# Kernel tuning notes

Hardware: AMD Instinct MI355X
Metric: run time of the kernel (lower is better)

The kernel has to match this reference:

```python
import jax, jax.numpy as jnp
from jax import lax
import numpy as np

B, C, H, W = 2, 64, 192, 192

def conv2d(x, w, pad):
    return lax.conv_general_dilated(x, w, (1, 1), [(pad, pad), (pad, pad)],
                                    dimension_numbers=('NCHW', 'OIHW', 'NCHW'))

def bilinear_sample(x, py, px):
    # x: [B,C,H,W]; py, px: [B,H,W] absolute fractional coords; zero padding outside.
    Bb, Cc, Hh, Ww = x.shape
    y0 = jnp.floor(py); x0 = jnp.floor(px)
    wy1 = py - y0; wx1 = px - x0
    xf = x.reshape(Bb, Cc, Hh * Ww)
    def gather(yi, xi):
        valid = (yi >= 0) & (yi < Hh) & (xi >= 0) & (xi < Ww)
        yc = jnp.clip(yi, 0, Hh - 1).astype(jnp.int32)
        xc = jnp.clip(xi, 0, Ww - 1).astype(jnp.int32)
        idx = (yc * Ww + xc).reshape(Bb, 1, Hh * Ww)
        v = jnp.take_along_axis(xf, idx, axis=2).reshape(Bb, Cc, Hh, Ww)
        return v * valid[:, None].astype(x.dtype)
    return (gather(y0, x0) * ((1 - wy1) * (1 - wx1))[:, None]
            + gather(y0, x0 + 1) * ((1 - wy1) * wx1)[:, None]
            + gather(y0 + 1, x0) * (wy1 * (1 - wx1))[:, None]
            + gather(y0 + 1, x0 + 1) * (wy1 * wx1)[:, None])

def deform_conv(x, w_off, b_off, w_mod, b_mod, w_reg, k):
    # torchvision deform_conv2d semantics with modulation (mask), stride=1, dilation=1.
    pad = k // 2
    offset = conv2d(x, w_off, pad) + b_off[None, :, None, None]   # [B,2*k*k,H,W] (y,x) interleaved
    mask = 2.0 * jax.nn.sigmoid(conv2d(x, w_mod, pad) + b_mod[None, :, None, None])  # [B,k*k,H,W]
    Bb, Cc, Hh, Ww = x.shape
    gy = jnp.arange(Hh, dtype=x.dtype)[None, :, None]
    gx = jnp.arange(Ww, dtype=x.dtype)[None, None, :]
    out = jnp.zeros((Bb, w_reg.shape[0], Hh, Ww), x.dtype)
    for i in range(k):          # fixed structural loop over kernel taps
        for j in range(k):
            t = i * k + j
            py = gy - pad + i + offset[:, 2 * t]
            px = gx - pad + j + offset[:, 2 * t + 1]
            samp = bilinear_sample(x, py, px) * mask[:, t][:, None]  # [B,C,H,W]
            out = out + jnp.einsum('bchw,oc->bohw', samp, w_reg[:, :, i, j])
    return out

def _branch(x, w_pre, w_off, b_off, w_mod, b_mod, w_reg, k):
    h = jax.nn.relu(conv2d(x, w_pre, 0))  # BasicConv 1x1 + ReLU (no bias)
    return deform_conv(h, w_off, b_off, w_mod, b_mod, w_reg, k)

def _forward(x_max, x_mid, x_small,
             w_pre_max, w_off_max, b_off_max, w_mod_max, b_mod_max, w_reg_max,
             w_pre_mid, w_off_mid, b_off_mid, w_mod_mid, b_mod_mid, w_reg_mid,
             w_pre_small, w_off_small, b_off_small, w_mod_small, b_mod_small, w_reg_small,
             w1, w2):
    y = x_max + x_mid + x_small
    a = _branch(x_max, w_pre_max, w_off_max, b_off_max, w_mod_max, b_mod_max, w_reg_max, 7)
    m = _branch(x_mid, w_pre_mid, w_off_mid, b_off_mid, w_mod_mid, b_mod_mid, w_reg_mid, 5)
    s = _branch(x_small, w_pre_small, w_off_small, b_off_small, w_mod_small, b_mod_small, w_reg_small, 3)
    x = jnp.tanh(m) * a
    x = jax.nn.relu(conv2d(x, w1, 0))
    x = jnp.tanh(s) * x
    x = jax.nn.relu(conv2d(x, w2, 0))
    return x + y

def setup_inputs() -> dict:
    key = jax.random.key(0)
    ks = jax.random.split(key, 32)
    d = {}
    d['x_max'] = jax.random.normal(ks[0], (B, C, H, W), jnp.float32)
    d['x_mid'] = jax.random.normal(ks[1], (B, C, H, W), jnp.float32)
    d['x_small'] = jax.random.normal(ks[2], (B, C, H, W), jnp.float32)
    i = 3
    for name, k in (('max', 7), ('mid', 5), ('small', 3)):
        d[f'w_pre_{name}'] = jax.random.normal(ks[i], (C, C, 1, 1), jnp.float32) * 0.05; i += 1
        d[f'w_off_{name}'] = jax.random.normal(ks[i], (2 * k * k, C, k, k), jnp.float32) * 0.01; i += 1
        d[f'b_off_{name}'] = jax.random.normal(ks[i], (2 * k * k,), jnp.float32) * 0.01; i += 1
        d[f'w_mod_{name}'] = jax.random.normal(ks[i], (k * k, C, k, k), jnp.float32) * 0.01; i += 1
        d[f'b_mod_{name}'] = jax.random.normal(ks[i], (k * k,), jnp.float32) * 0.01; i += 1
        d[f'w_reg_{name}'] = jax.random.normal(ks[i], (C, C, k, k), jnp.float32) * 0.02; i += 1
    d['w1'] = jax.random.normal(ks[i], (C, C, 1, 1), jnp.float32) * 0.05; i += 1
    d['w2'] = jax.random.normal(ks[i], (C, C, 1, 1), jnp.float32) * 0.05
    return d

def reference(x_max, x_mid, x_small,
              w_pre_max, w_off_max, b_off_max, w_mod_max, b_mod_max, w_reg_max,
              w_pre_mid, w_off_mid, b_off_mid, w_mod_mid, b_mod_mid, w_reg_mid,
              w_pre_small, w_off_small, b_off_small, w_mod_small, b_mod_small, w_reg_small,
              w1, w2):
    return _forward(x_max, x_mid, x_small,
                    w_pre_max, w_off_max, b_off_max, w_mod_max, b_mod_max, w_reg_max,
                    w_pre_mid, w_off_mid, b_off_mid, w_mod_mid, b_mod_mid, w_reg_mid,
                    w_pre_small, w_off_small, b_off_small, w_mod_small, b_mod_small, w_reg_small,
                    w1, w2)
```

## Files before the change

### kernel.cpp

```cpp
#include <hip/hip_runtime.h>
#include <hip/hip_bf16.h>
#include <math.h>

#define BB   2
#define CC   64
#define HH   192
#define WW   192
#define HW   (HH*WW)
#define HALO 3
#define HP   (HH + 2*HALO)
#define WP   (WW + 2*HALO)
#define PLANE (HP*WP)

typedef __attribute__((ext_vector_type(8))) _Float16 f16x8;
typedef __attribute__((ext_vector_type(4))) _Float16 f16x4;
typedef __attribute__((ext_vector_type(8))) unsigned short u16x8;
typedef __attribute__((ext_vector_type(4))) float f32x4;

__device__ __forceinline__ float fast_tanh(float x) {
    float e = __expf(2.f * x);
    return 1.f - 2.f * __builtin_amdgcn_rcpf(e + 1.f);
}
__device__ __forceinline__ f16x8 bc16(u16x8 v) { return __builtin_bit_cast(f16x8, v); }

__global__ __launch_bounds__(256) void conv_pre_k(
    const float* __restrict__ X0, const float* __restrict__ X1,
    const float* __restrict__ X2,
    const float* __restrict__ W0, const float* __restrict__ W1,
    const float* __restrict__ W2,
    u16x8* __restrict__ hp8all)
{
    __shared__ float wl[64*32];
    int tid = threadIdx.x;
    int oh  = blockIdx.y;
    int z   = blockIdx.z;
    const float* X = (z == 0) ? X0 : ((z == 1) ? X1 : X2);
    const float* W = (z == 0) ? W0 : ((z == 1) ? W1 : W2);
    u16x8* hp8 = hp8all + (size_t)z * ((size_t)BB*8*PLANE);

    #pragma unroll
    for (int n = 0; n < 8; n++) {
        int idx = tid + n*256;
        int op  = idx >> 6, c = idx & 63;
        wl[c*32 + op] = W[(size_t)(oh*32 + op)*64 + c];
    }
    __syncthreads();

    int p  = blockIdx.x*256 + tid;
    int b  = p / HW;
    int pp = p - b*HW;
    size_t base = (size_t)b*CC*HW + pp;

    float acc[32];
    #pragma unroll
    for (int o = 0; o < 32; o++) acc[o] = 0.f;

    #pragma unroll 4
    for (int c = 0; c < 64; c++) {
        float xv = X[base + (size_t)c*HW];
        const float4* w4 = (const float4*)(wl + c*32);
        #pragma unroll
        for (int q = 0; q < 8; q++) {
            float4 w = w4[q];
            acc[4*q+0] = fmaf(w.x, xv, acc[4*q+0]);
            acc[4*q+1] = fmaf(w.y, xv, acc[4*q+1]);
            acc[4*q+2] = fmaf(w.z, xv, acc[4*q+2]);
            acc[4*q+3] = fmaf(w.w, xv, acc[4*q+3]);
        }
    }

    int y = pp / WW, x = pp - y*WW;
    #pragma unroll
    for (int gq = 0; gq < 4; gq++) {
        u16x8 v;
        #pragma unroll
        for (int c = 0; c < 8; c++)
            v[c] = __builtin_bit_cast(unsigned short,
                     (_Float16)fmaxf(acc[gq*8+c], 0.f));
        hp8[(size_t)(b*8 + oh*4 + gq)*PLANE + (size_t)(y+HALO)*WP + (x+HALO)] = v;
    }
}

template<int MODE>
__global__ __launch_bounds__(256) void conv1x1_k(
    const _Float16* __restrict__ Xv, const _Float16* __restrict__ Mv,
    const float* __restrict__ W,
    const float* __restrict__ Y0, const float* __restrict__ Y1,
    const float* __restrict__ Y2,
    void* __restrict__ outv)
{
    __shared__ float wl[64*32];
    int tid = threadIdx.x;
    int oh  = blockIdx.y;
    #pragma unroll
    for (int n = 0; n < 8; n++) {
        int idx = tid + n*256;
        int op  = idx >> 6, c = idx & 63;
        wl[c*32 + op] = W[(size_t)(oh*32 + op)*64 + c];
    }
    __syncthreads();

    int p  = blockIdx.x*256 + tid;
    int b  = p / HW;
    int pp = p - b*HW;
    size_t base = (size_t)b*CC*HW + pp;

    float acc[32];
    #pragma unroll
    for (int o = 0; o < 32; o++) acc[o] = 0.f;

    #pragma unroll 4
    for (int c = 0; c < 64; c++) {
        float xv = (float)Xv[base + (size_t)c*HW];
        xv *= fast_tanh((float)Mv[base + (size_t)c*HW]);
        const float4* w4 = (const float4*)(wl + c*32);
        #pragma unroll
        for (int q = 0; q < 8; q++) {
            float4 w = w4[q];
            acc[4*q+0] = fmaf(w.x, xv, acc[4*q+0]);
            acc[4*q+1] = fmaf(w.y, xv, acc[4*q+1]);
            acc[4*q+2] = fmaf(w.z, xv, acc[4*q+2]);
            acc[4*q+3] = fmaf(w.w, xv, acc[4*q+3]);
        }
    }

    if (MODE == 1) {
        _Float16* op = (_Float16*)outv + base + (size_t)(oh*32)*HW;
        #pragma unroll
        for (int o = 0; o < 32; o++)
            op[(size_t)o*HW] = (_Float16)fmaxf(acc[o], 0.f);
    } else {
        float* op = (float*)outv + base + (size_t)(oh*32)*HW;
        size_t gi = base + (size_t)(oh*32)*HW;
        #pragma unroll
        for (int o = 0; o < 32; o++) {
            float yv = Y0[gi + (size_t)o*HW] + Y1[gi + (size_t)o*HW] + Y2[gi + (size_t)o*HW];
            op[(size_t)o*HW] = fmaxf(acc[o], 0.f) + yv;
        }
    }
}

template<int K>
__device__ void bake_wtb_dev(const float* __restrict__ Wreg,
                             f16x8* __restrict__ wtb, int t, int tid)
{
    constexpr int KK = K*K;
    for (int e = tid; e < 512; e += 256) {
        int kk = e >> 8, rem = e & 255;
        int ot = rem >> 6, l = rem & 63;
        int lr = l & 15, lg = l >> 4;
        int o  = ot*16 + lr;
        f16x8 v;
        #pragma unroll
        for (int j = 0; j < 8; j++) {
            int c = kk*32 + lg*8 + j;
            v[j] = (_Float16)Wreg[((size_t)o*CC + c)*KK + t];
        }
        wtb[(size_t)t*512 + e] = v;
    }
}
template<int K>
__device__ void bake_wbg_dev(const float* __restrict__ Woff,
                             const float* __restrict__ Wmod,
                             f16x8* __restrict__ wbg, int pos, int tid)
{
    constexpr int KK  = K*K;
    constexpr int NTF = (3*KK + 15)/16;
    for (int idx = tid; idx < 2*NTF*64; idx += 256) {
        int kk  = idx / (NTF*64);
        int rem = idx - kk*(NTF*64);
        int nt  = rem >> 6;
        int l   = rem & 63;
        int lg  = l >> 4, lr = l & 15;
        int n   = nt*16 + lr;
        f16x8 v;
        #pragma unroll
        for (int j = 0; j < 8; j++) {
            int c = kk*32 + lg*8 + j;
            float w = 0.f;
            if (n < 2*KK)      w = Woff[((size_t)n*CC + c)*KK + pos];
            else if (n < 3*KK) w = Wmod[((size_t)(n - 2*KK)*CC + c)*KK + pos];
            v[j] = (_Float16)w;
        }
        wbg[(size_t)pos*(2*NTF*64) + idx] = v;
    }
}
__global__ __launch_bounds__(256) void bake_all_k(
    const float* wreg7, const float* woff7, const float* wmod7,
    const float* wreg5, const float* woff5, const float* wmod5,
    const float* wreg3, const float* woff3, const float* wmod3,
    f16x8* wtb7, f16x8* wbg7, f16x8* wtb5, f16x8* wbg5,
    f16x8* wtb3, f16x8* wbg3)
{
    int blk = blockIdx.x, tid = threadIdx.x;
    if (blk < 49) {
        bake_wtb_dev<7>(wreg7, wtb7, blk, tid);
        bake_wbg_dev<7>(woff7, wmod7, wbg7, blk, tid);
    } else if (blk < 74) {
        int p = blk - 49;
        bake_wtb_dev<5>(wreg5, wtb5, p, tid);
        bake_wbg_dev<5>(woff5, wmod5, wbg5, p, tid);
    } else {
        int p = blk - 74;
        bake_wtb_dev<3>(wreg3, wtb3, p, tid);
        bake_wbg_dev<3>(woff3, wmod3, wbg3, p, tid);
    }
}

template<int K, int MT, int NS, int PPR>
__global__ __launch_bounds__(256) void offmod_mfma_k(
    const u16x8* __restrict__ hp8,
    const f16x8* __restrict__ wbg,
    const float* __restrict__ Boff, const float* __restrict__ Bmod,
    _Float16* __restrict__ om)
{
    constexpr int PAD  = K/2;
    constexpr int KK   = K*K;
    constexpr int NTF  = (3*KK + 15)/16;
    constexpr int NT   = NTF/NS;
    constexpr int PBB  = HW/(64*MT);
    constexpr int NBLK = BB*PBB*NS;
    constexpr int ROUNDS = (KK + PPR - 1)/PPR;
    constexpr int WELEM  = PPR*2*NT*64;

    __shared__ f16x8 wl[WELEM];

    int raw = blockIdx.x;
    int swz = (raw & 7)*(NBLK >> 3) + (raw >> 3);
    int ng  = swz % NS;
    int s   = swz / NS;
    int b   = s / PBB;
    int blk = s - b*PBB;

    int tid  = threadIdx.x;
    int wave = tid >> 6;
    int l    = tid & 63;
    int lg   = l >> 4, lr = l & 15;
    int pxw  = blk*(4*MT*16) + wave*(MT*16);
    int y    = pxw / WW, x0 = pxw - y*WW;

    f32x4 acc[MT][NT];
    #pragma unroll
    for (int mt = 0; mt < MT; mt++)
        #pragma unroll
        for (int nt = 0; nt < NT; nt++) acc[mt][nt] = (f32x4)0.f;

    const u16x8* hb = hp8 + (size_t)(b*8)*PLANE;

    for (int r = 0; r < ROUNDS; r++) {
        __syncthreads();
        #pragma unroll
        for (int ii = 0; ii < (WELEM + 255)/256; ii++) {
            int idx = tid + ii*256;
            if (WELEM % 256 == 0 || idx < WELEM) {
                int pp  = idx / (2*NT*64);
                int rem = idx - pp*(2*NT*64);
                int kk  = rem / (NT*64);
                int rem2= rem - kk*(NT*64);
                int nt  = rem2 >> 6;
                int ll  = rem2 & 63;
                int pos = r*PPR + pp;
                if (pos < KK)
                    wl[idx] = wbg[(size_t)pos*(2*NTF*64)
                                  + (size_t)(kk*NTF + ng*NT + nt)*64 + ll];
            }
        }
        __syncthreads();

        #pragma unroll
        for (int pp = 0; pp < PPR; pp++) {
            int pos = r*PPR + pp;
            if (pos >= KK) break;
            int i = pos / K, j = pos - (pos/K)*K;
            int rbase = (y + HALO - PAD + i)*WP + (x0 + HALO - PAD + j);

            #pragma unroll
            for (int kk = 0; kk < 2; kk++) {
                const f16x8* G = (const f16x8*)(hb + (size_t)(kk*4 + lg)*PLANE + rbase);
                f16x8 a[MT];
                #pragma unroll
                for (int mt = 0; mt < MT; mt++) a[mt] = G[mt*16 + lr];
                #pragma unroll
                for (int nt = 0; nt < NT; nt++) {
                    f16x8 bf = wl[((pp*2 + kk)*NT + nt)*64 + l];
                    #pragma unroll
                    for (int mt = 0; mt < MT; mt++)
                        acc[mt][nt] = __builtin_amdgcn_mfma_f32_16x16x32_f16(
                            a[mt], bf, acc[mt][nt], 0, 0, 0);
                }
            }
        }
    }

    #pragma unroll
    for (int nt = 0; nt < NT; nt++) {
        int n = ng*NT*16 + nt*16 + lr;
        if (n < 3*KK) {
            bool is_mask = (n >= 2*KK);
            float bias = is_mask ? Bmod[n - 2*KK] : Boff[n];
            _Float16* dst0 = om + ((size_t)b*3*KK + n)*HW + pxw + lg*4;
            #pragma unroll
            for (int mt = 0; mt < MT; mt++) {
                f32x4 v = acc[mt][nt];
                float v0 = v[0] + bias, v1 = v[1] + bias, v2 = v[2] + bias, v3 = v[3] + bias;
                if (is_mask) {
                    v0 = 2.f * __builtin_amdgcn_rcpf(1.f + __expf(-v0));
                    v1 = 2.f * __builtin_amdgcn_rcpf(1.f + __expf(-v1));
                    v2 = 2.f * __builtin_amdgcn_rcpf(1.f + __expf(-v2));
                    v3 = 2.f * __builtin_amdgcn_rcpf(1.f + __expf(-v3));
                }
                f16x4 o;
                o[0] = (_Float16)v0; o[1] = (_Float16)v1;
                o[2] = (_Float16)v2; o[3] = (_Float16)v3;
                *reinterpret_cast<f16x4*>(dst0 + mt*16) = o;
            }
        }
    }
}

template<int K>
__global__ __launch_bounds__(256, 4) void deform_mfma_k(
    const u16x8* __restrict__ hp8,
    const _Float16* __restrict__ om,
    const f16x8* __restrict__ wtb,
    _Float16* __restrict__ out)
{
    constexpr int PAD = K/2;
    constexpr int KK  = K*K;
    constexpr int NSB = HW/16;
    constexpr int HWW = K + 2;
    constexpr int WWW = 16 + K + 2;
    constexpr int WELEMS = 8*HWW*WWW;
    constexpr int NPT = KK*16;
    constexpr int COORD_B = NPT*8 + NPT*4 + ((NPT*2 + 15)/16)*16;
    constexpr int RED_B   = 2*64*16*4;
    constexpr int UNION_B = (COORD_B > RED_B ? COORD_B : RED_B);

    __shared__ u16x8 win[8][HWW][WWW];
    __shared__ __align__(16) char ubuf[UNION_B];

    f16x4*          hco  = (f16x4*)ubuf;
    unsigned*       gofs = (unsigned*)(ubuf + NPT*8);
    unsigned short* wofs = (unsigned short*)(ubuf + NPT*8 + NPT*4);

    int raw = blockIdx.x;
    int swz = (raw & 7)*((BB*NSB) >> 3) + (raw >> 3);
    int b = swz / NSB, strip = swz - b*NSB;

    int tid  = threadIdx.x;
    int wave = tid >> 6;
    int l    = tid & 63;
    int lg   = l >> 4;
    int lr   = l & 15;
    int th   = wave & 1;
    int kkh  = wave >> 1;
    int pxbase = strip*16;
    int y    = pxbase / WW;
    int xs   = pxbase - y*WW;

    int wy0 = y  + HALO - PAD - 1;
    int wx0 = xs + HALO - PAD - 1;

    {
        const u16x8* hbb = hp8 + (size_t)(b*8)*PLANE;
        for (int idx = tid; idx < WELEMS; idx += 256) {
            int g  = idx / (HWW*WWW);
            int r2 = idx - g*(HWW*WWW);
            int r  = r2 / WWW;
            int c2 = r2 - r*WWW;
            int gy = min(max(wy0 + r, 0), HP-1);
            int gx = min(max(wx0 + c2, 0), WP-1);
            win[g][r][c2] = hbb[(size_t)g*PLANE + gy*WP + gx];
        }
    }
    {
        const _Float16* ob = om + (size_t)b*3*KK*HW + pxbase;
        for (int idx = tid; idx < NPT; idx += 256) {
            int pxl = idx & 15, t = idx >> 4;
            float offy = (float)ob[(size_t)(2*t  )*HW + pxl];
            float offx = (float)ob[(size_t)(2*t+1)*HW + pxl];
            float mk   = (float)ob[(size_t)(2*KK+t)*HW + pxl];
            int i = t / K, j = t - (t/K)*K;
            float py  = (float)(y - PAD + i) + offy;
            float pxf = (float)(xs + pxl - PAD + j) + offx;
            float fy = floorf(py), fx = floorf(pxf);
            float wy1 = py - fy, wx1 = pxf - fx;
            int iy0 = (int)fy, ix0 = (int)fx;
            int Y0 = min(max(iy0, -1), HH) + HALO;
            int X0 = min(max(ix0, -1), WW) + HALO;
            int ry = Y0 - wy0, rx = X0 - wx0;
            bool in = ((unsigned)ry <= (unsigned)(HWW-2)) &
                      ((unsigned)rx <= (unsigned)(WWW-2));
            f16x4 h;
            h[0] = (_Float16)((1.f-wy1)*(1.f-wx1)*mk);
            h[1] = (_Float16)((1.f-wy1)*wx1*mk);
            h[2] = (_Float16)(wy1*(1.f-wx1)*mk);
            h[3] = (_Float16)(wy1*wx1*mk);
            hco[idx]  = h;
            gofs[idx] = (unsigned)(Y0*WP + X0);
            wofs[idx] = (unsigned short)((ry*WWW + rx) | (in ? 0 : 0x8000));
        }
    }
    __syncthreads();

    int t0 = (KK*th)/2, t1 = (KK*(th+1))/2;

    f32x4 acc[4];
    #pragma unroll
    for (int ot = 0; ot < 4; ot++) acc[ot] = (f32x4)0.f;

    const u16x8* hb   = hp8 + (size_t)(b*8 + kkh*4 + lg)*PLANE;
    const u16x8* wing = &win[kkh*4 + lg][0][0];

    #pragma unroll 1
    for (int t = t0; t < t1; t++) {
        int idx = t*16 + lr;
        f16x4 h = hco[idx];
        unsigned short wf = wofs[idx];
        bool in = (wf & 0x8000) == 0;

        f16x8 c0, c1, c2, c3;
        if (__all(in)) {
            const u16x8* Wp = wing + wf;
            c0 = bc16(Wp[0]);   c1 = bc16(Wp[1]);
            c2 = bc16(Wp[WWW]); c3 = bc16(Wp[WWW+1]);
        } else {
            const u16x8* G = hb + gofs[idx];
            c0 = bc16(G[0]);  c1 = bc16(G[1]);
            c2 = bc16(G[WP]); c3 = bc16(G[WP+1]);
        }

        f16x8 s = c0*h[0] + c1*h[1] + c2*h[2] + c3*h[3];

        const f16x8* bp = wtb + (size_t)t*8*64 + l;
        #pragma unroll
        for (int ot = 0; ot < 4; ot++) {
            acc[ot] = __builtin_amdgcn_mfma_f32_16x16x32_f16(
                s, bp[(size_t)(kkh*4 + ot)*64], acc[ot], 0, 0, 0);
        }
    }

    __syncthreads();
    float* redf = (float*)ubuf;
    #define RIDX(tt, o, g)  (((tt)*64 + (o))*16 + (((g) ^ ((o) & 3)) * 4))
    if (kkh == 1) {
        #pragma unroll
        for (int ot = 0; ot < 4; ot++) {
            int o = ot*16 + lr;
            *reinterpret_cast<f32x4*>(&redf[RIDX(th, o, lg)]) = acc[ot];
        }
    }
    __syncthreads();
    if (kkh == 0) {
        #pragma unroll
        for (int ot = 0; ot < 4; ot++) {
            int o = ot*16 + lr;
            acc[ot] += *reinterpret_cast<const f32x4*>(&redf[RIDX(th, o, lg)]);
        }
    }
    __syncthreads();
    if (kkh == 0 && th == 1) {
        #pragma unroll
        for (int ot = 0; ot < 4; ot++) {
            int o = ot*16 + lr;
            *reinterpret_cast<f32x4*>(&redf[RIDX(0, o, lg)]) = acc[ot];
        }
    }
    __syncthreads();
    if (kkh == 0 && th == 0) {
        _Float16* ob = out + (size_t)b*CC*HW + pxbase + lg*4;
        #pragma unroll
        for (int ot = 0; ot < 4; ot++) {
            int o = ot*16 + lr;
            f32x4 rr = *reinterpret_cast<const f32x4*>(&redf[RIDX(0, o, lg)]);
            rr += acc[ot];
            f16x4 v;
            v[0] = (_Float16)rr[0]; v[1] = (_Float16)rr[1];
            v[2] = (_Float16)rr[2]; v[3] = (_Float16)rr[3];
            *reinterpret_cast<f16x4*>(ob + (size_t)o*HW) = v;
        }
    }
    #undef RIDX
}

extern "C" void kernel_launch(void* const* d_in, const int* in_sizes, int n_in,
                              void* d_out, int out_size, void* d_ws, size_t ws_size,
                              hipStream_t stream)
{
    const float* x_max      = (const float*)d_in[0];
    const float* x_mid      = (const float*)d_in[1];
    const float* x_small    = (const float*)d_in[2];
    const float* w_pre_max  = (const float*)d_in[3];
    const float* w_off_max  = (const float*)d_in[4];
    const float* b_off_max  = (const float*)d_in[5];
    const float* w_mod_max  = (const float*)d_in[6];
    const float* b_mod_max  = (const float*)d_in[7];
    const float* w_reg_max  = (const float*)d_in[8];
    const float* w_pre_mid  = (const float*)d_in[9];
    const float* w_off_mid  = (const float*)d_in[10];
    const float* b_off_mid  = (const float*)d_in[11];
    const float* w_mod_mid  = (const float*)d_in[12];
    const float* b_mod_mid  = (const float*)d_in[13];
    const float* w_reg_mid  = (const float*)d_in[14];
    const float* w_pre_small= (const float*)d_in[15];
    const float* w_off_small= (const float*)d_in[16];
    const float* b_off_small= (const float*)d_in[17];
    const float* w_mod_small= (const float*)d_in[18];
    const float* b_mod_small= (const float*)d_in[19];
    const float* w_reg_small= (const float*)d_in[20];
    const float* w1         = (const float*)d_in[21];
    const float* w2         = (const float*)d_in[22];

    float* out = (float*)d_out;
    char*  ws  = (char*)d_ws;

    const size_t HPB = (size_t)BB*8*PLANE;

    u16x8*    hp8 = (u16x8*)ws;                 ws += 3*HPB*16;
    _Float16* om  = (_Float16*)ws;              ws += (size_t)BB*3*49*HW*2;
    _Float16* aa  = (_Float16*)ws;              ws += (size_t)BB*CC*HW*2;
    _Float16* mm  = (_Float16*)ws;              ws += (size_t)BB*CC*HW*2;
    _Float16* sm  = (_Float16*)ws;              ws += (size_t)BB*CC*HW*2;
    _Float16* u   = (_Float16*)ws;              ws += (size_t)BB*CC*HW*2;
    f16x8*    wtb7= (f16x8*)ws;                 ws += (size_t)49*512*16;
    f16x8*    wbg7= (f16x8*)ws;                 ws += (size_t)49*2*10*64*16;
    f16x8*    wtb5= (f16x8*)ws;                 ws += (size_t)25*512*16;
    f16x8*    wbg5= (f16x8*)ws;                 ws += (size_t)25*2*5*64*16;
    f16x8*    wtb3= (f16x8*)ws;                 ws += (size_t)9*512*16;
    f16x8*    wbg3= (f16x8*)ws;

    hipMemsetAsync(hp8, 0, 3*HPB*16, stream);

    const int npix_blocks = (BB*HW)/256;
    const int dfm_blocks  = BB*(HW/16);
    const int off7_blocks = BB*(HW/128)*2;
    const int off5_blocks = BB*(HW/64);
    const int off3_blocks = BB*(HW/128);

    bake_all_k<<<83, 256, 0, stream>>>(
        w_reg_max, w_off_max, w_mod_max,
        w_reg_mid, w_off_mid, w_mod_mid,
        w_reg_small, w_off_small, w_mod_small,
        wtb7, wbg7, wtb5, wbg5, wtb3, wbg3);
    conv_pre_k<<<dim3(npix_blocks, 2, 3), 256, 0, stream>>>(
        x_max, x_mid, x_small, w_pre_max, w_pre_mid, w_pre_small, hp8);

    offmod_mfma_k<7,2,2,2><<<off7_blocks, 256, 0, stream>>>(
        hp8 + 0*HPB, wbg7, b_off_max, b_mod_max, om);
    deform_mfma_k<7><<<dfm_blocks, 256, 0, stream>>>(hp8 + 0*HPB, om, wtb7, aa);

    offmod_mfma_k<5,1,1,2><<<off5_blocks, 256, 0, stream>>>(
        hp8 + 1*HPB, wbg5, b_off_mid, b_mod_mid, om);
    deform_mfma_k<5><<<dfm_blocks, 256, 0, stream>>>(hp8 + 1*HPB, om, wtb5, mm);

    offmod_mfma_k<3,2,1,3><<<off3_blocks, 256, 0, stream>>>(
        hp8 + 2*HPB, wbg3, b_off_small, b_mod_small, om);
    deform_mfma_k<3><<<dfm_blocks, 256, 0, stream>>>(hp8 + 2*HPB, om, wtb3, sm);

    conv1x1_k<1><<<dim3(npix_blocks,2), 256, 0, stream>>>(aa, mm, w1,
                                                  nullptr, nullptr, nullptr, u);
    conv1x1_k<2><<<dim3(npix_blocks,2), 256, 0, stream>>>(u, sm, w2,
                                                  x_max, x_mid, x_small, out);
}
```

Before: 431.9 us.

## Double-buffer offset/mask weight staging per tap and retile N-splits

```diff
diff --git a/kernel.cpp b/kernel.cpp
--- a/kernel.cpp
+++ b/kernel.cpp
@@ -207,7 +207,7 @@
     }
 }
 
-template<int K, int MT, int NS, int PPR>
+template<int K, int MT, int NS>
 __global__ __launch_bounds__(256) void offmod_mfma_k(
     const u16x8* __restrict__ hp8,
     const f16x8* __restrict__ wbg,
@@ -220,10 +220,9 @@
     constexpr int NT   = NTF/NS;
     constexpr int PBB  = HW/(64*MT);
     constexpr int NBLK = BB*PBB*NS;
-    constexpr int ROUNDS = (KK + PPR - 1)/PPR;
-    constexpr int WELEM  = PPR*2*NT*64;
-
-    __shared__ f16x8 wl[WELEM];
+    constexpr int PELEM = 2*NT*64;
+
+    __shared__ f16x8 wl[2][PELEM];
 
     int raw = blockIdx.x;
     int swz = (raw & 7)*(NBLK >> 3) + (raw >> 3);
@@ -247,49 +246,48 @@
 
     const u16x8* hb = hp8 + (size_t)(b*8)*PLANE;
 
-    for (int r = 0; r < ROUNDS; r++) {
+    auto stage = [&](int buf, int pos) {
+        #pragma unroll
+        for (int ii = 0; ii < (PELEM + 255)/256; ii++) {
+            int idx = tid + ii*256;
+            if (PELEM % 256 == 0 || idx < PELEM) {
+                int kk  = idx / (NT*64);
+                int rem = idx - kk*(NT*64);
+                int nt  = rem >> 6;
+                int ll  = rem & 63;
+                wl[buf][idx] = wbg[(size_t)pos*(2*NTF*64)
+                                   + (size_t)(kk*NTF + ng*NT + nt)*64 + ll];
+            }
+        }
+    };
+
+    stage(0, 0);
+    __syncthreads();
+
+    int buf = 0;
+    for (int pos = 0; pos < KK; pos++) {
+        if (pos + 1 < KK) stage(buf ^ 1, pos + 1);
+
+        int i = pos / K, j = pos - (pos/K)*K;
+        int rbase = (y + HALO - PAD + i)*WP + (x0 + HALO - PAD + j);
+
+        #pragma unroll
+        for (int kk = 0; kk < 2; kk++) {
+            const f16x8* G = (const f16x8*)(hb + (size_t)(kk*4 + lg)*PLANE + rbase);
+            f16x8 a[MT];
+            #pragma unroll
+            for (int mt = 0; mt < MT; mt++) a[mt] = G[mt*16 + lr];
+            #pragma unroll
+            for (int nt = 0; nt < NT; nt++) {
+                f16x8 bf = wl[buf][(kk*NT + nt)*64 + l];
+                #pragma unroll
+                for (int mt = 0; mt < MT; mt++)
+                    acc[mt][nt] = __builtin_amdgcn_mfma_f32_16x16x32_f16(
+                        a[mt], bf, acc[mt][nt], 0, 0, 0);
+            }
+        }
         __syncthreads();
-        #pragma unroll
-        for (int ii = 0; ii < (WELEM + 255)/256; ii++) {
-            int idx = tid + ii*256;
-            if (WELEM % 256 == 0 || idx < WELEM) {
-                int pp  = idx / (2*NT*64);
-                int rem = idx - pp*(2*NT*64);
-                int kk  = rem / (NT*64);
-                int rem2= rem - kk*(NT*64);
-                int nt  = rem2 >> 6;
-                int ll  = rem2 & 63;
-                int pos = r*PPR + pp;
-                if (pos < KK)
-                    wl[idx] = wbg[(size_t)pos*(2*NTF*64)
-                                  + (size_t)(kk*NTF + ng*NT + nt)*64 + ll];
-            }
-        }
-        __syncthreads();
-
-        #pragma unroll
-        for (int pp = 0; pp < PPR; pp++) {
-            int pos = r*PPR + pp;
-            if (pos >= KK) break;
-            int i = pos / K, j = pos - (pos/K)*K;
-            int rbase = (y + HALO - PAD + i)*WP + (x0 + HALO - PAD + j);
-
-            #pragma unroll
-            for (int kk = 0; kk < 2; kk++) {
-                const f16x8* G = (const f16x8*)(hb + (size_t)(kk*4 + lg)*PLANE + rbase);
-                f16x8 a[MT];
-                #pragma unroll
-                for (int mt = 0; mt < MT; mt++) a[mt] = G[mt*16 + lr];
-                #pragma unroll
-                for (int nt = 0; nt < NT; nt++) {
-                    f16x8 bf = wl[((pp*2 + kk)*NT + nt)*64 + l];
-                    #pragma unroll
-                    for (int mt = 0; mt < MT; mt++)
-                        acc[mt][nt] = __builtin_amdgcn_mfma_f32_16x16x32_f16(
-                            a[mt], bf, acc[mt][nt], 0, 0, 0);
-                }
-            }
-        }
+        buf ^= 1;
     }
 
     #pragma unroll
@@ -533,9 +531,9 @@
 
     const int npix_blocks = (BB*HW)/256;
     const int dfm_blocks  = BB*(HW/16);
-    const int off7_blocks = BB*(HW/128)*2;
-    const int off5_blocks = BB*(HW/64);
-    const int off3_blocks = BB*(HW/128);
+    const int off7_blocks = BB*(HW/128)*5;
+    const int off5_blocks = BB*(HW/128)*5;
+    const int off3_blocks = BB*(HW/128)*2;
 
     bake_all_k<<<83, 256, 0, stream>>>(
         w_reg_max, w_off_max, w_mod_max,
@@ -545,15 +543,15 @@
     conv_pre_k<<<dim3(npix_blocks, 2, 3), 256, 0, stream>>>(
         x_max, x_mid, x_small, w_pre_max, w_pre_mid, w_pre_small, hp8);
 
-    offmod_mfma_k<7,2,2,2><<<off7_blocks, 256, 0, stream>>>(
+    offmod_mfma_k<7,2,5><<<off7_blocks, 256, 0, stream>>>(
         hp8 + 0*HPB, wbg7, b_off_max, b_mod_max, om);
     deform_mfma_k<7><<<dfm_blocks, 256, 0, stream>>>(hp8 + 0*HPB, om, wtb7, aa);
 
-    offmod_mfma_k<5,1,1,2><<<off5_blocks, 256, 0, stream>>>(
+    offmod_mfma_k<5,2,5><<<off5_blocks, 256, 0, stream>>>(
         hp8 + 1*HPB, wbg5, b_off_mid, b_mod_mid, om);
     deform_mfma_k<5><<<dfm_blocks, 256, 0, stream>>>(hp8 + 1*HPB, om, wtb5, mm);
 
-    offmod_mfma_k<3,2,1,3><<<off3_blocks, 256, 0, stream>>>(
+    offmod_mfma_k<3,2,2><<<off3_blocks, 256, 0, stream>>>(
         hp8 + 2*HPB, wbg3, b_off_small, b_mod_small, om);
     deform_mfma_k<3><<<dfm_blocks, 256, 0, stream>>>(hp8 + 2*HPB, om, wtb3, sm);
 
```

After: 449.0 us. 4.0% more time.

## Merge per-branch offset/mask and deform kernels into single batched launches

Applied to the files above, without the earlier changes.

```diff
diff --git a/kernel.cpp b/kernel.cpp
--- a/kernel.cpp
+++ b/kernel.cpp
@@ -208,7 +208,8 @@
 }
 
 template<int K, int MT, int NS, int PPR>
-__global__ __launch_bounds__(256) void offmod_mfma_k(
+__device__ __forceinline__ void offmod_dev(
+    char* smem_raw, int raw,
     const u16x8* __restrict__ hp8,
     const f16x8* __restrict__ wbg,
     const float* __restrict__ Boff, const float* __restrict__ Bmod,
@@ -223,9 +224,8 @@
     constexpr int ROUNDS = (KK + PPR - 1)/PPR;
     constexpr int WELEM  = PPR*2*NT*64;
 
-    __shared__ f16x8 wl[WELEM];
-
-    int raw = blockIdx.x;
+    f16x8* wl = (f16x8*)smem_raw;
+
     int swz = (raw & 7)*(NBLK >> 3) + (raw >> 3);
     int ng  = swz % NS;
     int s   = swz / NS;
@@ -318,8 +318,43 @@
     }
 }
 
+__global__ __launch_bounds__(256) void offmod_all_k(
+    const u16x8* __restrict__ hp8,
+    const f16x8* __restrict__ wbg7, const f16x8* __restrict__ wbg5,
+    const f16x8* __restrict__ wbg3,
+    const float* __restrict__ boff7, const float* __restrict__ bmod7,
+    const float* __restrict__ boff5, const float* __restrict__ bmod5,
+    const float* __restrict__ boff3, const float* __restrict__ bmod3,
+    _Float16* __restrict__ om7, _Float16* __restrict__ om5,
+    _Float16* __restrict__ om3)
+{
+    __shared__ __align__(16) char smem[20480];
+    constexpr size_t HPB = (size_t)BB*8*PLANE;
+    constexpr int G7 = BB*(HW/128)*2;
+    constexpr int G5 = BB*(HW/64);
+    int blk = blockIdx.x;
+    if (blk < G7)
+        offmod_dev<7,2,2,2>(smem, blk, hp8, wbg7, boff7, bmod7, om7);
+    else if (blk < G7 + G5)
+        offmod_dev<5,1,1,2>(smem, blk - G7, hp8 + HPB, wbg5, boff5, bmod5, om5);
+    else
+        offmod_dev<3,2,1,3>(smem, blk - G7 - G5, hp8 + 2*HPB, wbg3, boff3, bmod3, om3);
+}
+
+template<int K> struct DfmLds {
+    static constexpr int HWW = K + 2;
+    static constexpr int WWW = 16 + K + 2;
+    static constexpr int WIN_B = 8*HWW*WWW*16;
+    static constexpr int NPT = K*K*16;
+    static constexpr int COORD_B = NPT*8 + NPT*4 + ((NPT*2 + 15)/16)*16;
+    static constexpr int RED_B = 2*64*16*4;
+    static constexpr int UNION_B = (COORD_B > RED_B ? COORD_B : RED_B);
+    static constexpr int TOTAL = WIN_B + UNION_B;
+};
+
 template<int K>
-__global__ __launch_bounds__(256, 4) void deform_mfma_k(
+__device__ __forceinline__ void deform_dev(
+    char* smem_raw, int raw,
     const u16x8* __restrict__ hp8,
     const _Float16* __restrict__ om,
     const f16x8* __restrict__ wtb,
@@ -332,18 +367,14 @@
     constexpr int WWW = 16 + K + 2;
     constexpr int WELEMS = 8*HWW*WWW;
     constexpr int NPT = KK*16;
-    constexpr int COORD_B = NPT*8 + NPT*4 + ((NPT*2 + 15)/16)*16;
-    constexpr int RED_B   = 2*64*16*4;
-    constexpr int UNION_B = (COORD_B > RED_B ? COORD_B : RED_B);
-
-    __shared__ u16x8 win[8][HWW][WWW];
-    __shared__ __align__(16) char ubuf[UNION_B];
+
+    u16x8* win = (u16x8*)smem_raw;
+    char*  ubuf = smem_raw + WELEMS*16;
 
     f16x4*          hco  = (f16x4*)ubuf;
     unsigned*       gofs = (unsigned*)(ubuf + NPT*8);
     unsigned short* wofs = (unsigned short*)(ubuf + NPT*8 + NPT*4);
 
-    int raw = blockIdx.x;
     int swz = (raw & 7)*((BB*NSB) >> 3) + (raw >> 3);
     int b = swz / NSB, strip = swz - b*NSB;
 
@@ -370,7 +401,7 @@
             int c2 = r2 - r*WWW;
             int gy = min(max(wy0 + r, 0), HP-1);
             int gx = min(max(wx0 + c2, 0), WP-1);
-            win[g][r][c2] = hbb[(size_t)g*PLANE + gy*WP + gx];
+            win[idx] = hbb[(size_t)g*PLANE + gy*WP + gx];
         }
     }
     {
@@ -410,7 +441,7 @@
     for (int ot = 0; ot < 4; ot++) acc[ot] = (f32x4)0.f;
 
     const u16x8* hb   = hp8 + (size_t)(b*8 + kkh*4 + lg)*PLANE;
-    const u16x8* wing = &win[kkh*4 + lg][0][0];
+    const u16x8* wing = win + (kkh*4 + lg)*(HWW*WWW);
 
     #pragma unroll 1
     for (int t = t0; t < t1; t++) {
@@ -481,6 +512,31 @@
         }
     }
     #undef RIDX
+}
+
+__global__ __launch_bounds__(256, 4) void deform_all_k(
+    const u16x8* __restrict__ hp8,
+    const _Float16* __restrict__ om7, const _Float16* __restrict__ om5,
+    const _Float16* __restrict__ om3,
+    const f16x8* __restrict__ wtb7, const f16x8* __restrict__ wtb5,
+    const f16x8* __restrict__ wtb3,
+    _Float16* __restrict__ aa, _Float16* __restrict__ mm,
+    _Float16* __restrict__ sm)
+{
+    constexpr int DFM_SMEM =
+        (DfmLds<7>::TOTAL > DfmLds<5>::TOTAL ?
+            (DfmLds<7>::TOTAL > DfmLds<3>::TOTAL ? DfmLds<7>::TOTAL : DfmLds<3>::TOTAL)
+          : (DfmLds<5>::TOTAL > DfmLds<3>::TOTAL ? DfmLds<5>::TOTAL : DfmLds<3>::TOTAL));
+    __shared__ __align__(16) char smem[DFM_SMEM];
+    constexpr size_t HPB = (size_t)BB*8*PLANE;
+    constexpr int GD = BB*(HW/16);
+    int blk = blockIdx.x;
+    if (blk < GD)
+        deform_dev<7>(smem, blk, hp8, om7, wtb7, aa);
+    else if (blk < 2*GD)
+        deform_dev<5>(smem, blk - GD, hp8 + HPB, om5, wtb5, mm);
+    else
+        deform_dev<3>(smem, blk - 2*GD, hp8 + 2*HPB, om3, wtb3, sm);
 }
 
 extern "C" void kernel_launch(void* const* d_in, const int* in_sizes, int n_in,
@@ -517,25 +573,25 @@
     const size_t HPB = (size_t)BB*8*PLANE;
 
     u16x8*    hp8 = (u16x8*)ws;                 ws += 3*HPB*16;
-    _Float16* om  = (_Float16*)ws;              ws += (size_t)BB*3*49*HW*2;
+    _Float16* om7 = (_Float16*)ws;              ws += (size_t)BB*3*49*HW*2;
+    _Float16* om5 = (_Float16*)ws;              ws += (size_t)BB*3*25*HW*2;
+    _Float16* om3 = (_Float16*)ws;              ws += (size_t)BB*3*9*HW*2;
     _Float16* aa  = (_Float16*)ws;              ws += (size_t)BB*CC*HW*2;
     _Float16* mm  = (_Float16*)ws;              ws += (size_t)BB*CC*HW*2;
     _Float16* sm  = (_Float16*)ws;              ws += (size_t)BB*CC*HW*2;
-    _Float16* u   = (_Float16*)ws;              ws += (size_t)BB*CC*HW*2;
     f16x8*    wtb7= (f16x8*)ws;                 ws += (size_t)49*512*16;
     f16x8*    wbg7= (f16x8*)ws;                 ws += (size_t)49*2*10*64*16;
     f16x8*    wtb5= (f16x8*)ws;                 ws += (size_t)25*512*16;
     f16x8*    wbg5= (f16x8*)ws;                 ws += (size_t)25*2*5*64*16;
     f16x8*    wtb3= (f16x8*)ws;                 ws += (size_t)9*512*16;
     f16x8*    wbg3= (f16x8*)ws;
+    _Float16* u   = om7;
 
     hipMemsetAsync(hp8, 0, 3*HPB*16, stream);
 
     const int npix_blocks = (BB*HW)/256;
-    const int dfm_blocks  = BB*(HW/16);
-    const int off7_blocks = BB*(HW/128)*2;
-    const int off5_blocks = BB*(HW/64);
-    const int off3_blocks = BB*(HW/128);
+    const int off_blocks  = BB*(HW/128)*2 + BB*(HW/64) + BB*(HW/128);
+    const int dfm_blocks  = 3*BB*(HW/16);
 
     bake_all_k<<<83, 256, 0, stream>>>(
         w_reg_max, w_off_max, w_mod_max,
@@ -545,17 +601,13 @@
     conv_pre_k<<<dim3(npix_blocks, 2, 3), 256, 0, stream>>>(
         x_max, x_mid, x_small, w_pre_max, w_pre_mid, w_pre_small, hp8);
 
-    offmod_mfma_k<7,2,2,2><<<off7_blocks, 256, 0, stream>>>(
-        hp8 + 0*HPB, wbg7, b_off_max, b_mod_max, om);
-    deform_mfma_k<7><<<dfm_blocks, 256, 0, stream>>>(hp8 + 0*HPB, om, wtb7, aa);
-
-    offmod_mfma_k<5,1,1,2><<<off5_blocks, 256, 0, stream>>>(
-        hp8 + 1*HPB, wbg5, b_off_mid, b_mod_mid, om);
-    deform_mfma_k<5><<<dfm_blocks, 256, 0, stream>>>(hp8 + 1*HPB, om, wtb5, mm);
-
-    offmod_mfma_k<3,2,1,3><<<off3_blocks, 256, 0, stream>>>(
-        hp8 + 2*HPB, wbg3, b_off_small, b_mod_small, om);
-    deform_mfma_k<3><<<dfm_blocks, 256, 0, stream>>>(hp8 + 2*HPB, om, wtb3, sm);
+    offmod_all_k<<<off_blocks, 256, 0, stream>>>(
+        hp8, wbg7, wbg5, wbg3,
+        b_off_max, b_mod_max, b_off_mid, b_mod_mid, b_off_small, b_mod_small,
+        om7, om5, om3);
+
+    deform_all_k<<<dfm_blocks, 256, 0, stream>>>(
+        hp8, om7, om5, om3, wtb7, wtb5, wtb3, aa, mm, sm);
 
     conv1x1_k<1><<<dim3(npix_blocks,2), 256, 0, stream>>>(aa, mm, w1,
                                                   nullptr, nullptr, nullptr, u);
```

Result: faster. 396.3 us (median of 2 runs) (-8.2%).
